# Kernel tuning notes

Hardware: AMD Instinct MI355X
Metric: run time of the kernel (lower is better)

## Reference

```python
import jax, jax.numpy as jnp
import numpy as np

PARENTS = np.array([0, 0, 1, 2, 3, 0, 5, 6, 7, 0, 9, 10, 11, 12, 11, 14, 15, 16, 11, 18, 19, 20])
SPARSE_JOINTS = [0, 4, 8, 13, 17, 21]
EE = np.array(SPARSE_JOINTS[1:])                       # end effectors (skip root)
NO_SPARSE = np.array([i for i in range(22) if i not in SPARSE_JOINTS])
LAMBDA_EE = 1.0
LAMBDA_EE_REG = 0.1
IDENT_DQ = np.array([1, 0, 0, 0, 0, 0, 0, 0], dtype=np.float32)


def qmul(a, b):
    # Hamilton product, (w, x, y, z) convention
    aw, ax, ay, az = a[..., 0], a[..., 1], a[..., 2], a[..., 3]
    bw, bx, by, bz = b[..., 0], b[..., 1], b[..., 2], b[..., 3]
    return jnp.stack([
        aw * bw - ax * bx - ay * by - az * bz,
        aw * bx + ax * bw + ay * bz - az * by,
        aw * by - ax * bz + ay * bw + az * bx,
        aw * bz + ax * by - ay * bx + az * bw,
    ], axis=-1)


def qconj(q):
    return q * jnp.array([1.0, -1.0, -1.0, -1.0], dtype=q.dtype)


def quat_to_matrix(q, eps=1e-8):
    # normalize then convert to 3x3 rotation matrix
    q = q / jnp.maximum(jnp.linalg.norm(q, axis=-1, keepdims=True), eps)
    w, x, y, z = q[..., 0], q[..., 1], q[..., 2], q[..., 3]
    m = jnp.stack([
        1 - 2 * (y * y + z * z), 2 * (x * y - w * z), 2 * (x * z + w * y),
        2 * (x * y + w * z), 1 - 2 * (x * x + z * z), 2 * (y * z - w * x),
        2 * (x * z - w * y), 2 * (y * z + w * x), 1 - 2 * (x * x + y * y),
    ], axis=-1)
    return m.reshape(q.shape[:-1] + (3, 3))


def denorm_reshape(d, mean, std, set_root):
    # d: (B, 176, T) -> (B, T, 22, 8)
    d = d * std[None, :, None] + mean[None, :, None]
    if set_root:
        d = d.at[:, :8, :].set(jnp.asarray(IDENT_DQ)[None, :, None])
    B, C, T = d.shape
    return d.reshape(B, C // 8, 8, T).transpose(0, 3, 1, 2)


def local_rots(dq):
    # from_root_dual_quat: local_q[j] = conj(global_q[parent[j]]) * global_q[j]
    # (parents always have lower index than children so the original reversed
    # sequential loop reads untouched parent globals -> fully vectorizable)
    qr = dq[..., :4]                       # (B, T, 22, 4) real part
    loc = qmul(qconj(qr[..., PARENTS, :]), qr)
    # root local rotation forced to identity (as in forward_ik)
    return loc.at[..., 0, :].set(jnp.array([1.0, 0.0, 0.0, 0.0], dtype=dq.dtype))


def fk(local_rot, root_pos, offsets):
    # local_rot: (B, T, J, 4); root_pos: (B, T, 3); offsets: (J, 3)
    mats = quat_to_matrix(local_rot)       # (B, T, J, 3, 3)
    gmats = [mats[..., 0, :, :]]
    gpos = [root_pos]
    for j in range(1, PARENTS.shape[0]):   # fixed 22-joint skeleton walk
        p = int(PARENTS[j])
        gmats.append(jnp.matmul(gmats[p], mats[..., j, :, :]))
        gpos.append(jnp.einsum('btij,j->bti', gmats[p], offsets[j]) + gpos[p])
    return jnp.stack(gpos, axis=2), jnp.stack(gmats, axis=2)


def mse(a, b):
    return jnp.mean(jnp.square(a - b))


def setup_inputs() -> dict:
    key = jax.random.key(0)
    ks = jax.random.split(key, 7)
    B, T, J = 32, 4096, 22
    return {
        'input': jax.random.normal(ks[0], (1, 1), dtype=jnp.float32),
        'input_ik': jax.random.normal(ks[1], (B, (J - 1) * 8, T), dtype=jnp.float32),
        'input_decoder': jax.random.normal(ks[2], (B, J * 8, T), dtype=jnp.float32),
        'target': jax.random.normal(ks[3], (B, J * 8, T), dtype=jnp.float32),
        'mean_dqs': jax.random.normal(ks[4], (J * 8,), dtype=jnp.float32) * 0.1,
        'std_dqs': jax.random.uniform(ks[5], (J * 8,), dtype=jnp.float32, minval=0.5, maxval=1.5),
        'offsets': jax.random.normal(ks[6], (J, 3), dtype=jnp.float32),
    }


def reference(input, input_ik, input_decoder, target, mean_dqs, std_dqs, offsets):
    B, _, T = input_ik.shape
    # pad root dq channels with zeros (then overwritten by identity dq)
    dqs = jnp.concatenate([jnp.zeros((B, 8, T), input_ik.dtype), input_ik], axis=1)
    dqs = denorm_reshape(dqs, mean_dqs, std_dqs, set_root=True)            # (B,T,22,8)
    dqs_dec = denorm_reshape(input_decoder, mean_dqs, std_dqs, set_root=True)
    dqs_tgt = denorm_reshape(target, mean_dqs, std_dqs, set_root=False)

    rot_ik = local_rots(dqs)
    rot_dec = local_rots(dqs_dec)
    rot_tgt = local_rots(dqs_tgt)

    root_pos = jnp.zeros((B, T, 3), dtype=input_ik.dtype)
    pos_ik, mat_ik = fk(rot_ik, root_pos, offsets)
    pos_tgt, mat_tgt = fk(rot_tgt, root_pos, offsets)
    pos_dec, mat_dec = fk(rot_dec, root_pos, offsets)

    loss_ee = mse(pos_ik[:, :, EE, :], pos_tgt[:, :, EE, :])
    loss_ee += mse(mat_ik[:, :, EE, :, :], mat_tgt[:, :, EE, :, :])
    loss_reg = mse(pos_dec[:, :, NO_SPARSE, :], pos_ik[:, :, NO_SPARSE, :])
    loss_reg += mse(mat_dec[:, :, NO_SPARSE, :, :], mat_ik[:, :, NO_SPARSE, :, :])
    return loss_ee * LAMBDA_EE + loss_reg * LAMBDA_EE_REG
```

## Files before the change

kernel.cpp:

```cpp
#include <hip/hip_runtime.h>

#define TDIM 4096
#define SBAR() __builtin_amdgcn_sched_barrier(0)

__device__ __forceinline__ void fk_step(float* __restrict__ f,
                                        const float* __restrict__ q,
                                        float o0, float o1, float o2) {
  const float pw = f[12], px = f[13], py = f[14], pz = f[15];
  float lw = pw*q[0] + px*q[1] + py*q[2] + pz*q[3];
  float lx = pw*q[1] - px*q[0] - py*q[3] + pz*q[2];
  float ly = pw*q[2] + px*q[3] - py*q[0] - pz*q[1];
  float lz = pw*q[3] - px*q[2] + py*q[1] - pz*q[0];
  float n2 = lw*lw + lx*lx + ly*ly + lz*lz;
  float inv = rsqrtf(fmaxf(n2, 1e-16f));
  lw *= inv; lx *= inv; ly *= inv; lz *= inv;
  float xx = lx*lx, yy = ly*ly, zz = lz*lz;
  float xy = lx*ly, xz = lx*lz, yz = ly*lz;
  float wx = lw*lx, wy = lw*ly, wz = lw*lz;
  float m0 = 1.0f-2.0f*(yy+zz), m1 = 2.0f*(xy-wz),      m2 = 2.0f*(xz+wy);
  float m3 = 2.0f*(xy+wz),      m4 = 1.0f-2.0f*(xx+zz), m5 = 2.0f*(yz-wx);
  float m6 = 2.0f*(xz-wy),      m7 = 2.0f*(yz+wx),      m8 = 1.0f-2.0f*(xx+yy);
  f[9]  += f[0]*o0 + f[1]*o1 + f[2]*o2;
  f[10] += f[3]*o0 + f[4]*o1 + f[5]*o2;
  f[11] += f[6]*o0 + f[7]*o1 + f[8]*o2;
  float r0 = f[0]*m0 + f[1]*m3 + f[2]*m6;
  float r1 = f[0]*m1 + f[1]*m4 + f[2]*m7;
  float r2 = f[0]*m2 + f[1]*m5 + f[2]*m8;
  float r3 = f[3]*m0 + f[4]*m3 + f[5]*m6;
  float r4 = f[3]*m1 + f[4]*m4 + f[5]*m7;
  float r5 = f[3]*m2 + f[4]*m5 + f[5]*m8;
  float r6 = f[6]*m0 + f[7]*m3 + f[8]*m6;
  float r7 = f[6]*m1 + f[7]*m4 + f[8]*m7;
  float r8 = f[6]*m2 + f[7]*m5 + f[8]*m8;
  f[0]=r0; f[1]=r1; f[2]=r2; f[3]=r3; f[4]=r4; f[5]=r5; f[6]=r6; f[7]=r7; f[8]=r8;
  f[12]=q[0]; f[13]=q[1]; f[14]=q[2]; f[15]=q[3];
}

__global__ __launch_bounds__(256, 4) void fk_loss_kernel(
    const float* __restrict__ ik,
    const float* __restrict__ dec,
    const float* __restrict__ tgt,
    const float* __restrict__ mean,
    const float* __restrict__ stdv,
    const float* __restrict__ offs,
    float* __restrict__ out)
{
  __shared__ float s_mean[176];
  __shared__ float s_std[176];
  __shared__ float s_save[36 * 256];
  __shared__ float s_wsum[4];
  const int tid = threadIdx.x;
  for (int i = tid; i < 176; i += 256) { s_mean[i] = mean[i]; s_std[i] = stdv[i]; }
  __syncthreads();

  const int idx = blockIdx.x * 256 + tid;
  const int b = idx >> 12;
  const int t = idx & 4095;
  const float* __restrict__ pik  = ik  + ((size_t)b * 168) * TDIM + t;
  const float* __restrict__ pdec = dec + ((size_t)b * 176) * TDIM + t;
  const float* __restrict__ ptgt = tgt + ((size_t)b * 176) * TDIM + t;

  float see_p = 0.f, see_m = 0.f, srg_p = 0.f, srg_m = 0.f;

  float fik[16], fdec[16], ftgt[16];
  float rq[4];
  float qsv[12];
  float A[12], B[12];

#define LOADST(buf, j)                                                         \
  { _Pragma("unroll")                                                          \
    for (int c = 0; c < 4; c++) buf[c]      = pik [(((j)-1)*8 + c) * TDIM];    \
    _Pragma("unroll")                                                          \
    for (int c = 0; c < 4; c++) buf[4 + c]  = pdec[(((j)*8)   + c) * TDIM];    \
    _Pragma("unroll")                                                          \
    for (int c = 0; c < 4; c++) buf[8 + c]  = ptgt[(((j)*8)   + c) * TDIM]; }

#define COMP(buf, j, IS_EE)                                                    \
  { float qi[4], qd[4], qt[4];                                                 \
    _Pragma("unroll")                                                          \
    for (int c = 0; c < 4; c++) {                                              \
      const float sd = s_std[(j)*8 + c], mn = s_mean[(j)*8 + c];               \
      qi[c] = fmaf(buf[c],     sd, mn);                                        \
      qd[c] = fmaf(buf[4+c],   sd, mn);                                        \
      qt[c] = fmaf(buf[8+c],   sd, mn);                                        \
    }                                                                          \
    const float o0 = offs[(j)*3], o1 = offs[(j)*3+1], o2 = offs[(j)*3+2];      \
    fk_step(fik,  qi, o0, o1, o2);                                             \
    fk_step(fdec, qd, o0, o1, o2);                                             \
    fk_step(ftgt, qt, o0, o1, o2);                                             \
    if (IS_EE) {                                                               \
      _Pragma("unroll")                                                        \
      for (int c = 0; c < 3; c++) { float d = fik[9+c] - ftgt[9+c]; see_p = fmaf(d, d, see_p); } \
      _Pragma("unroll")                                                        \
      for (int c = 0; c < 9; c++) { float d = fik[c]   - ftgt[c];   see_m = fmaf(d, d, see_m); } \
    } else {                                                                   \
      _Pragma("unroll")                                                        \
      for (int c = 0; c < 3; c++) { float d = fdec[9+c] - fik[9+c]; srg_p = fmaf(d, d, srg_p); } \
      _Pragma("unroll")                                                        \
      for (int c = 0; c < 9; c++) { float d = fdec[c]   - fik[c];   srg_m = fmaf(d, d, srg_m); } \
    } }

#define RESET()                                                                \
  { _Pragma("unroll")                                                          \
    for (int c = 0; c < 16; c++) { fik[c] = 0.f; fdec[c] = 0.f; ftgt[c] = 0.f; } \
    fik[0]=fik[4]=fik[8]=1.f; fdec[0]=fdec[4]=fdec[8]=1.f; ftgt[0]=ftgt[4]=ftgt[8]=1.f; \
    fik[12]=1.f; fdec[12]=1.f;                                                 \
    ftgt[12]=rq[0]; ftgt[13]=rq[1]; ftgt[14]=rq[2]; ftgt[15]=rq[3]; }

#define SAVE()                                                                 \
  { _Pragma("unroll")                                                          \
    for (int c = 0; c < 12; c++) {                                             \
      s_save[c*256 + tid]      = fik[c];                                       \
      s_save[(12+c)*256 + tid] = fdec[c];                                      \
      s_save[(24+c)*256 + tid] = ftgt[c];                                      \
    }                                                                          \
    _Pragma("unroll")                                                          \
    for (int c = 0; c < 4; c++) { qsv[c]=fik[12+c]; qsv[4+c]=fdec[12+c]; qsv[8+c]=ftgt[12+c]; } }

#define RESTORE()                                                              \
  { _Pragma("unroll")                                                          \
    for (int c = 0; c < 12; c++) {                                             \
      fik[c]  = s_save[c*256 + tid];                                           \
      fdec[c] = s_save[(12+c)*256 + tid];                                      \
      ftgt[c] = s_save[(24+c)*256 + tid];                                      \
    }                                                                          \
    _Pragma("unroll")                                                          \
    for (int c = 0; c < 4; c++) { fik[12+c]=qsv[c]; fdec[12+c]=qsv[4+c]; ftgt[12+c]=qsv[8+c]; } }

  float rqr[4];
  #pragma unroll
  for (int c = 0; c < 4; c++) rqr[c] = ptgt[c * TDIM];
  LOADST(A, 1);
  SBAR();
  #pragma unroll
  for (int c = 0; c < 4; c++) rq[c] = fmaf(rqr[c], s_std[c], s_mean[c]);
  RESET();
  LOADST(B, 2);  COMP(A, 1,  false); SBAR();
  LOADST(A, 3);  COMP(B, 2,  false); SBAR();
  LOADST(B, 4);  COMP(A, 3,  false); SBAR();
  LOADST(A, 5);  COMP(B, 4,  true);  RESET(); SBAR();
  LOADST(B, 6);  COMP(A, 5,  false); SBAR();
  LOADST(A, 7);  COMP(B, 6,  false); SBAR();
  LOADST(B, 8);  COMP(A, 7,  false); SBAR();
  LOADST(A, 9);  COMP(B, 8,  true);  RESET(); SBAR();
  LOADST(B, 10); COMP(A, 9,  false); SBAR();
  LOADST(A, 11); COMP(B, 10, false); SBAR();
  LOADST(B, 12); COMP(A, 11, false); SAVE(); SBAR();
  LOADST(A, 13); COMP(B, 12, false); SBAR();
  LOADST(B, 14); COMP(A, 13, true);  RESTORE(); SBAR();
  LOADST(A, 15); COMP(B, 14, false); SBAR();
  LOADST(B, 16); COMP(A, 15, false); SBAR();
  LOADST(A, 17); COMP(B, 16, false); SBAR();
  LOADST(B, 18); COMP(A, 17, true);  RESTORE(); SBAR();
  LOADST(A, 19); COMP(B, 18, false); SBAR();
  LOADST(B, 20); COMP(A, 19, false); SBAR();
  LOADST(A, 21); COMP(B, 20, false); SBAR();
  COMP(A, 21, true);

#undef LOADST
#undef COMP
#undef RESET
#undef SAVE
#undef RESTORE

  const float W1 = 1.0f / 1966080.0f;
  const float W2 = 1.0f / 5898240.0f;
  const float W3 = 0.1f / 6291456.0f;
  const float W4 = 0.1f / 18874368.0f;
  float val = see_p * W1 + see_m * W2 + srg_p * W3 + srg_m * W4;

  #pragma unroll
  for (int o = 32; o > 0; o >>= 1) val += __shfl_down(val, o, 64);
  const int wid = tid >> 6, lane = tid & 63;
  if (lane == 0) s_wsum[wid] = val;
  __syncthreads();
  if (tid == 0) atomicAdd(out, s_wsum[0] + s_wsum[1] + s_wsum[2] + s_wsum[3]);
}

extern "C" void kernel_launch(void* const* d_in, const int* in_sizes, int n_in,
                              void* d_out, int out_size, void* d_ws, size_t ws_size,
                              hipStream_t stream) {
  const float* ik   = (const float*)d_in[1];
  const float* dec  = (const float*)d_in[2];
  const float* tgt  = (const float*)d_in[3];
  const float* mean = (const float*)d_in[4];
  const float* stdv = (const float*)d_in[5];
  const float* offs = (const float*)d_in[6];
  float* out = (float*)d_out;

  hipMemsetAsync(out, 0, sizeof(float), stream);
  fk_loss_kernel<<<dim3(512), dim3(256), 0, stream>>>(ik, dec, tgt, mean, stdv, offs, out);
}
```

Measured before the change: 35.38 us.

## Triple-buffer joint loads and keep saved FK state in registers

```diff
diff --git a/kernel.cpp b/kernel.cpp
--- a/kernel.cpp
+++ b/kernel.cpp
@@ -36,7 +36,7 @@
   f[12]=q[0]; f[13]=q[1]; f[14]=q[2]; f[15]=q[3];
 }
 
-__global__ __launch_bounds__(256, 4) void fk_loss_kernel(
+__global__ __launch_bounds__(256) void fk_loss_kernel(
     const float* __restrict__ ik,
     const float* __restrict__ dec,
     const float* __restrict__ tgt,
@@ -47,7 +47,6 @@
 {
   __shared__ float s_mean[176];
   __shared__ float s_std[176];
-  __shared__ float s_save[36 * 256];
   __shared__ float s_wsum[4];
   const int tid = threadIdx.x;
   for (int i = tid; i < 176; i += 256) { s_mean[i] = mean[i]; s_std[i] = stdv[i]; }
@@ -63,9 +62,9 @@
   float see_p = 0.f, see_m = 0.f, srg_p = 0.f, srg_m = 0.f;
 
   float fik[16], fdec[16], ftgt[16];
+  float sik[16], sdec[16], stgt[16];
   float rq[4];
-  float qsv[12];
-  float A[12], B[12];
+  float A[12], B[12], C[12];
 
 #define LOADST(buf, j)                                                         \
   { _Pragma("unroll")                                                          \
@@ -109,53 +108,42 @@
 
 #define SAVE()                                                                 \
   { _Pragma("unroll")                                                          \
-    for (int c = 0; c < 12; c++) {                                             \
-      s_save[c*256 + tid]      = fik[c];                                       \
-      s_save[(12+c)*256 + tid] = fdec[c];                                      \
-      s_save[(24+c)*256 + tid] = ftgt[c];                                      \
-    }                                                                          \
-    _Pragma("unroll")                                                          \
-    for (int c = 0; c < 4; c++) { qsv[c]=fik[12+c]; qsv[4+c]=fdec[12+c]; qsv[8+c]=ftgt[12+c]; } }
+    for (int c = 0; c < 16; c++) { sik[c]=fik[c]; sdec[c]=fdec[c]; stgt[c]=ftgt[c]; } }
 
 #define RESTORE()                                                              \
   { _Pragma("unroll")                                                          \
-    for (int c = 0; c < 12; c++) {                                             \
-      fik[c]  = s_save[c*256 + tid];                                           \
-      fdec[c] = s_save[(12+c)*256 + tid];                                      \
-      ftgt[c] = s_save[(24+c)*256 + tid];                                      \
-    }                                                                          \
-    _Pragma("unroll")                                                          \
-    for (int c = 0; c < 4; c++) { fik[12+c]=qsv[c]; fdec[12+c]=qsv[4+c]; ftgt[12+c]=qsv[8+c]; } }
+    for (int c = 0; c < 16; c++) { fik[c]=sik[c]; fdec[c]=sdec[c]; ftgt[c]=stgt[c]; } }
 
   float rqr[4];
   #pragma unroll
   for (int c = 0; c < 4; c++) rqr[c] = ptgt[c * TDIM];
   LOADST(A, 1);
+  LOADST(B, 2);
   SBAR();
   #pragma unroll
   for (int c = 0; c < 4; c++) rq[c] = fmaf(rqr[c], s_std[c], s_mean[c]);
   RESET();
-  LOADST(B, 2);  COMP(A, 1,  false); SBAR();
-  LOADST(A, 3);  COMP(B, 2,  false); SBAR();
-  LOADST(B, 4);  COMP(A, 3,  false); SBAR();
-  LOADST(A, 5);  COMP(B, 4,  true);  RESET(); SBAR();
-  LOADST(B, 6);  COMP(A, 5,  false); SBAR();
-  LOADST(A, 7);  COMP(B, 6,  false); SBAR();
-  LOADST(B, 8);  COMP(A, 7,  false); SBAR();
-  LOADST(A, 9);  COMP(B, 8,  true);  RESET(); SBAR();
-  LOADST(B, 10); COMP(A, 9,  false); SBAR();
-  LOADST(A, 11); COMP(B, 10, false); SBAR();
-  LOADST(B, 12); COMP(A, 11, false); SAVE(); SBAR();
-  LOADST(A, 13); COMP(B, 12, false); SBAR();
-  LOADST(B, 14); COMP(A, 13, true);  RESTORE(); SBAR();
-  LOADST(A, 15); COMP(B, 14, false); SBAR();
-  LOADST(B, 16); COMP(A, 15, false); SBAR();
-  LOADST(A, 17); COMP(B, 16, false); SBAR();
-  LOADST(B, 18); COMP(A, 17, true);  RESTORE(); SBAR();
-  LOADST(A, 19); COMP(B, 18, false); SBAR();
-  LOADST(B, 20); COMP(A, 19, false); SBAR();
-  LOADST(A, 21); COMP(B, 20, false); SBAR();
-  COMP(A, 21, true);
+  LOADST(C, 3);  COMP(A, 1,  false); SBAR();
+  LOADST(A, 4);  COMP(B, 2,  false); SBAR();
+  LOADST(B, 5);  COMP(C, 3,  false); SBAR();
+  LOADST(C, 6);  COMP(A, 4,  true);  RESET(); SBAR();
+  LOADST(A, 7);  COMP(B, 5,  false); SBAR();
+  LOADST(B, 8);  COMP(C, 6,  false); SBAR();
+  LOADST(C, 9);  COMP(A, 7,  false); SBAR();
+  LOADST(A, 10); COMP(B, 8,  true);  RESET(); SBAR();
+  LOADST(B, 11); COMP(C, 9,  false); SBAR();
+  LOADST(C, 12); COMP(A, 10, false); SBAR();
+  LOADST(A, 13); COMP(B, 11, false); SAVE(); SBAR();
+  LOADST(B, 14); COMP(C, 12, false); SBAR();
+  LOADST(C, 15); COMP(A, 13, true);  RESTORE(); SBAR();
+  LOADST(A, 16); COMP(B, 14, false); SBAR();
+  LOADST(B, 17); COMP(C, 15, false); SBAR();
+  LOADST(C, 18); COMP(A, 16, false); SBAR();
+  LOADST(A, 19); COMP(B, 17, true);  RESTORE(); SBAR();
+  LOADST(B, 20); COMP(C, 18, false); SBAR();
+  LOADST(C, 21); COMP(A, 19, false); SBAR();
+  COMP(B, 20, false); SBAR();
+  COMP(C, 21, true);
 
 #undef LOADST
 #undef COMP
```

New measurement: 34.62 us. 2.2% less time.
